# Kernel optimization log

Hardware: AMD Instinct MI355X
Metric: run time of the kernel (lower is better)

The kernel has to match this reference:

```python
import jax, jax.numpy as jnp
import numpy as np

B, H, L, D = 2, 32, 4096, 128   # max_batch_size, n_heads, max_cache_length, head_dim
T = 2048                         # prefill length
G = 4                            # global_tokens


def setup_inputs() -> dict:
    key = jax.random.key(0)
    ks = jax.random.split(key, 5)
    return {
        "k_cache": jnp.zeros((B, H, L, D), jnp.float32),
        "v_cache": jnp.zeros((B, H, L, D), jnp.float32),
        "pos": jnp.full((B, H, L), -1, jnp.int32),            # -1 sentinel as in __init__
        "input_pos": jnp.arange(T, dtype=jnp.int32),           # prefill positions 0..T-1
        "k_val": jax.random.normal(ks[0], (B, H, T, D), jnp.float32),
        "v_val": jax.random.normal(ks[1], (B, H, T, D), jnp.float32),
        "fill_indices": jax.random.randint(ks[2], (H,), 0, L, jnp.int32),  # per-head slot
        "k_step": jax.random.normal(ks[3], (B, H, 1, D), jnp.float32),
        "v_step": jax.random.normal(ks[4], (B, H, 1, D), jnp.float32),
        "input_pos_step": T,                                    # decode token position
    }


def reference(k_cache, v_cache, pos, input_pos, k_val, v_val,
              fill_indices, k_step, v_step, input_pos_step):
    # ---- fill_contiguous (prefill): write k/v into [start:start+T], start = cache_cts = 0
    k_cache = jax.lax.dynamic_update_slice(k_cache, k_val, (0, 0, 0, 0))
    v_cache = jax.lax.dynamic_update_slice(v_cache, v_val, (0, 0, 0, 0))
    pos = pos.at[:, :, :T].set(input_pos[None, None, :])
    # ---- mark_global_tokens: global slots get highest priority (= max_cache_length)
    pos = pos.at[:, :, :G].set(jnp.int32(L))
    # ---- fill_headwise (decode step): per-head scatter of one token at fill_indices
    h = jnp.arange(H)
    k_cache = k_cache.at[:, h, fill_indices, :].set(k_step[:, :, 0, :])
    v_cache = v_cache.at[:, h, fill_indices, :].set(v_step[:, :, 0, :])
    pos = pos.at[:, h, fill_indices].set(jnp.int32(input_pos_step))
    return k_cache, v_cache, pos
```

## Files before the change

kernel.cpp:

```cpp
#include <hip/hip_runtime.h>


typedef float f4 __attribute__((ext_vector_type(4)));

__global__ __launch_bounds__(256) void kv_copy(
    const f4* __restrict__ k_cache, const f4* __restrict__ v_cache,
    const f4* __restrict__ k_val,   const f4* __restrict__ v_val,
    f4* __restrict__ outK, f4* __restrict__ outV)
{
    const int total  = 8388608;
    const int stride = gridDim.x * blockDim.x;
    int i = blockIdx.x * blockDim.x + threadIdx.x;
#pragma unroll 4
    for (; i < total; i += stride) {
        const int w  = i & 131071;
        f4 kv, vv;
        if (w < 65536) {
            const int s = ((i >> 17) << 16) + w;
            kv = __builtin_nontemporal_load(&k_val[s]);
            vv = __builtin_nontemporal_load(&v_val[s]);
        } else {
            kv = __builtin_nontemporal_load(&k_cache[i]);
            vv = __builtin_nontemporal_load(&v_cache[i]);
        }
        __builtin_nontemporal_store(kv, &outK[i]);
        __builtin_nontemporal_store(vv, &outV[i]);
    }
}

__global__ __launch_bounds__(256) void fixup(
    const int* __restrict__ pos_in,
    const int* __restrict__ input_pos,
    const int* __restrict__ fill_indices,
    const int* __restrict__ input_pos_step,
    const f4* __restrict__ k_step, const f4* __restrict__ v_step,
    f4* __restrict__ outK, f4* __restrict__ outV, float* __restrict__ outPos)
{
    const int i = blockIdx.x * blockDim.x + threadIdx.x;
    if (i < 262144) {
        const int l = i & 4095;
        const int h = (i >> 12) & 31;
        const int fi = fill_indices[h];
        int p;
        if (l == fi)        p = input_pos_step[0];
        else if (l < 4)     p = 4096;
        else if (l < 2048)  p = input_pos[l];
        else                p = pos_in[i];
        outPos[i] = (float)p;
    } else if (i < 262144 + 2048) {
        const int j  = i - 262144;
        const int bh = j >> 5;
        const int d4 = j & 31;
        const int fi = fill_indices[bh & 31];
        const int s  = (bh << 5) + d4;
        const int o  = (bh << 17) + (fi << 5) + d4;
        outK[o] = k_step[s];
        outV[o] = v_step[s];
    }
}

extern "C" void kernel_launch(void* const* d_in, const int* in_sizes, int n_in,
                              void* d_out, int out_size, void* d_ws, size_t ws_size,
                              hipStream_t stream) {
    const float* k_cache = (const float*)d_in[0];
    const float* v_cache = (const float*)d_in[1];
    const int*   pos_in  = (const int*)d_in[2];
    const int*   input_pos = (const int*)d_in[3];
    const float* k_val   = (const float*)d_in[4];
    const float* v_val   = (const float*)d_in[5];
    const int*   fill_indices = (const int*)d_in[6];
    const float* k_step  = (const float*)d_in[7];
    const float* v_step  = (const float*)d_in[8];
    const int*   input_pos_step = (const int*)d_in[9];

    const long KC = 33554432;
    float* outK = (float*)d_out;
    float* outV = outK + KC;
    float* outPos = outV + KC;

    kv_copy<<<2048, 256, 0, stream>>>(
        (const f4*)k_cache, (const f4*)v_cache,
        (const f4*)k_val,   (const f4*)v_val,
        (f4*)outK, (f4*)outV);

    fixup<<<(262144 + 2048 + 255) / 256, 256, 0, stream>>>(
        pos_in, input_pos, fill_indices, input_pos_step,
        (const f4*)k_step, (const f4*)v_step,
        (f4*)outK, (f4*)outV, outPos);
}
```

Baseline: 489.2 us.

## Fuse KV copy, decode scatter and pos fixup into one kernel

Merges the bulk KV copy and the fixup kernel into a single launch. Each copy block handles a contiguous 4096-vector chunk and selects the decode-step token inline when the row equals the fill index, so the later overwrite of outK/outV goes away. 64 extra blocks compute the pos output. This drops a kernel launch and the serialized write-after-write dependency, at the cost of a per-element branch on fill_indices in the copy loop.

New measurement: 512.3 us. 1.05x slower.

```diff
diff --git a/kernel.cpp b/kernel.cpp
--- a/kernel.cpp
+++ b/kernel.cpp
@@ -3,59 +3,58 @@
 
 typedef float f4 __attribute__((ext_vector_type(4)));
 
-__global__ __launch_bounds__(256) void kv_copy(
+__global__ __launch_bounds__(256) void kv_fused(
     const f4* __restrict__ k_cache, const f4* __restrict__ v_cache,
     const f4* __restrict__ k_val,   const f4* __restrict__ v_val,
-    f4* __restrict__ outK, f4* __restrict__ outV)
-{
-    const int total  = 8388608;
-    const int stride = gridDim.x * blockDim.x;
-    int i = blockIdx.x * blockDim.x + threadIdx.x;
-#pragma unroll 4
-    for (; i < total; i += stride) {
-        const int w  = i & 131071;
-        f4 kv, vv;
-        if (w < 65536) {
-            const int s = ((i >> 17) << 16) + w;
-            kv = __builtin_nontemporal_load(&k_val[s]);
-            vv = __builtin_nontemporal_load(&v_val[s]);
-        } else {
-            kv = __builtin_nontemporal_load(&k_cache[i]);
-            vv = __builtin_nontemporal_load(&v_cache[i]);
-        }
-        __builtin_nontemporal_store(kv, &outK[i]);
-        __builtin_nontemporal_store(vv, &outV[i]);
-    }
-}
-
-__global__ __launch_bounds__(256) void fixup(
-    const int* __restrict__ pos_in,
-    const int* __restrict__ input_pos,
     const int* __restrict__ fill_indices,
+    const f4* __restrict__ k_step,  const f4* __restrict__ v_step,
+    const int* __restrict__ pos_in, const int* __restrict__ input_pos,
     const int* __restrict__ input_pos_step,
-    const f4* __restrict__ k_step, const f4* __restrict__ v_step,
     f4* __restrict__ outK, f4* __restrict__ outV, float* __restrict__ outPos)
 {
-    const int i = blockIdx.x * blockDim.x + threadIdx.x;
-    if (i < 262144) {
-        const int l = i & 4095;
-        const int h = (i >> 12) & 31;
-        const int fi = fill_indices[h];
-        int p;
-        if (l == fi)        p = input_pos_step[0];
-        else if (l < 4)     p = 4096;
-        else if (l < 2048)  p = input_pos[l];
-        else                p = pos_in[i];
-        outPos[i] = (float)p;
-    } else if (i < 262144 + 2048) {
-        const int j  = i - 262144;
-        const int bh = j >> 5;
-        const int d4 = j & 31;
-        const int fi = fill_indices[bh & 31];
-        const int s  = (bh << 5) + d4;
-        const int o  = (bh << 17) + (fi << 5) + d4;
-        outK[o] = k_step[s];
-        outV[o] = v_step[s];
+    const int b = blockIdx.x;
+    if (b < 2048) {
+        const int base = b << 12;
+        const int bh   = base >> 17;
+        const int fi   = fill_indices[bh & 31];
+        const int sstep = bh << 5;
+#pragma unroll
+        for (int it = 0; it < 16; ++it) {
+            const int i  = base + (it << 8) + (int)threadIdx.x;
+            const int w  = i & 131071;
+            const int l  = w >> 5;
+            f4 kv, vv;
+            if (l == fi) {
+                const int s = sstep + (i & 31);
+                kv = k_step[s];
+                vv = v_step[s];
+            } else if (w < 65536) {
+                const int s = (bh << 16) + w;
+                kv = __builtin_nontemporal_load(&k_val[s]);
+                vv = __builtin_nontemporal_load(&v_val[s]);
+            } else {
+                kv = __builtin_nontemporal_load(&k_cache[i]);
+                vv = __builtin_nontemporal_load(&v_cache[i]);
+            }
+            __builtin_nontemporal_store(kv, &outK[i]);
+            __builtin_nontemporal_store(vv, &outV[i]);
+        }
+    } else {
+        const int bh    = b - 2048;
+        const int pbase = bh << 12;
+        const int fi    = fill_indices[bh & 31];
+        const int ps    = input_pos_step[0];
+#pragma unroll
+        for (int it = 0; it < 16; ++it) {
+            const int idx = pbase + (it << 8) + (int)threadIdx.x;
+            const int l   = idx & 4095;
+            int p;
+            if (l == fi)        p = ps;
+            else if (l < 4)     p = 4096;
+            else if (l < 2048)  p = input_pos[l];
+            else                p = pos_in[idx];
+            outPos[idx] = (float)p;
+        }
     }
 }
 
@@ -78,13 +77,11 @@
     float* outV = outK + KC;
     float* outPos = outV + KC;
 
-    kv_copy<<<2048, 256, 0, stream>>>(
+    kv_fused<<<2048 + 64, 256, 0, stream>>>(
         (const f4*)k_cache, (const f4*)v_cache,
         (const f4*)k_val,   (const f4*)v_val,
-        (f4*)outK, (f4*)outV);
-
-    fixup<<<(262144 + 2048 + 255) / 256, 256, 0, stream>>>(
-        pos_in, input_pos, fill_indices, input_pos_step,
-        (const f4*)k_step, (const f4*)v_step,
+        fill_indices,
+        (const f4*)k_step,  (const f4*)v_step,
+        pos_in, input_pos, input_pos_step,
         (f4*)outK, (f4*)outV, outPos);
 }
```
